# Optimization experiments

Hardware: AMD Instinct MI355X
Metric: run time of the kernel (lower is better)

Reference implementation:

```python
import jax, jax.numpy as jnp
import numpy as np

B, T, D, U = 32, 2048, 1024, 1024

def setup_inputs() -> dict:
    key = jax.random.key(0)
    ks = jax.random.split(key, 8)
    s = 0.02
    return {
        "query": jax.random.normal(ks[0], (B, D), dtype=jnp.float32),
        "values": jax.random.normal(ks[1], (B, T, D), dtype=jnp.float32),
        "W1": jax.random.normal(ks[2], (D, U), dtype=jnp.float32) * s,
        "b1": jnp.zeros((U,), dtype=jnp.float32),
        "W2": jax.random.normal(ks[3], (D, U), dtype=jnp.float32) * s,
        "b2": jnp.zeros((U,), dtype=jnp.float32),
        "V": jax.random.normal(ks[4], (U, 1), dtype=jnp.float32) * s,
        "bv": jnp.zeros((1,), dtype=jnp.float32),
    }

def reference(query, values, W1, b1, W2, b2, V, bv):
    # query: [B, D] -> [B, 1, U] via W2; values: [B, T, D] -> [B, T, U] via W1
    q_proj = query @ W2 + b2                     # [B, U]
    v_proj = jnp.einsum('btd,du->btu', values, W1) + b1   # [B, T, U]
    # score: Dense(1) on tanh(sum) -> [B, T, 1]
    score = jnp.tanh(v_proj + q_proj[:, None, :]) @ V + bv  # [B, T, 1]
    attention_weights = jax.nn.softmax(score, axis=1)        # softmax over time
    context_vector = jnp.sum(attention_weights * values, axis=1)  # [B, D]
    return context_vector, attention_weights
```

## Files before the change

kernel.cpp:

```cpp
#include <hip/hip_runtime.h>
#include <hip/hip_bf16.h>
#include <stdint.h>

#define WS_W1F   0
#define WS_QP2   2097152
#define WS_ESC   (WS_QP2 + 131072)
#define WS_PCTX  (WS_ESC + 262144)
#define WS_PDEN  (WS_PCTX + 4194304)
#define WS_NEED  (WS_PDEN + 4096)

typedef __attribute__((ext_vector_type(8))) short bf16x8;
typedef __attribute__((ext_vector_type(4))) float f32x4;

__device__ inline uint16_t f2b(float f) {
    __hip_bfloat16 h = __float2bfloat16(f);
    return *reinterpret_cast<uint16_t*>(&h);
}

__global__ __launch_bounds__(256) void k_prep(const float* __restrict__ W1,
                                              const float* __restrict__ query,
                                              const float* __restrict__ W2,
                                              const float* __restrict__ b1,
                                              const float* __restrict__ b2,
                                              __hip_bfloat16* __restrict__ W1f,
                                              float* __restrict__ qp2,
                                              float* __restrict__ zctx,
                                              float* __restrict__ zden) {
    __shared__ float qs[1024];
    __shared__ float part[4][64];
    int blk = blockIdx.x, tid = threadIdx.x;
    if (blk < 256) {
        int lane = tid & 63, fi = tid >> 6;
        int l15 = lane & 15, quad = lane >> 4;
        #pragma unroll
        for (int p = 0; p < 2; ++p) {
            int frag = blk * 8 + p * 4 + fi;
            int ut = frag >> 5, ks = frag & 31;
            union { uint16_t h[8]; int4 v; } pk;
            #pragma unroll
            for (int j = 0; j < 8; ++j) {
                float x = W1[(size_t)(ks * 32 + quad * 8 + j) * 1024 + ut * 16 + l15];
                pk.h[j] = f2b(x);
            }
            *(int4*)((char*)W1f + (size_t)frag * 1024 + lane * 16) = pk.v;
        }
    } else {
        int bq = blk - 256;
        int b = bq >> 4, us = bq & 15, u0 = us * 64;
        if (zctx != nullptr && us == 0) {
            *(float4*)(zctx + b * 1024 + tid * 4) = make_float4(0.f, 0.f, 0.f, 0.f);
            if (b == 0 && tid < 32) zden[tid] = 0.f;
        }
        const float* q = query + b * 1024;
        #pragma unroll
        for (int i = 0; i < 4; ++i) qs[i * 256 + tid] = q[i * 256 + tid];
        __syncthreads();
        int ul = tid & 63, g = tid >> 6;
        float a = 0.f;
        const float* w2p = W2 + (size_t)(g * 256) * 1024 + u0 + ul;
        const float* qg = qs + g * 256;
        #pragma unroll 8
        for (int d = 0; d < 256; ++d)
            a += qg[d] * w2p[(size_t)d * 1024];
        part[g][ul] = a;
        __syncthreads();
        if (tid < 64) {
            float r = part[0][tid] + part[1][tid] + part[2][tid] + part[3][tid]
                    + b1[u0 + tid] + b2[u0 + tid];
            qp2[b * 1024 + u0 + tid] = r;
        }
    }
}

__global__ __launch_bounds__(512, 1) void k_score(
        const float* __restrict__ values, const __hip_bfloat16* __restrict__ W1f,
        const float* __restrict__ qp2, const float* __restrict__ V,
        float* __restrict__ escore, float* __restrict__ pctx,
        float* __restrict__ pden, float* __restrict__ ctxa) {
    extern __shared__ char smem[];
    uint16_t* Al = (uint16_t*)smem;
    float* red = (float*)(smem + 131072);

    const int tid = threadIdx.x;
    const int lane = tid & 63, w = tid >> 6;
    const int quad = lane >> 4, l15 = lane & 15;
    const int b = blockIdx.x >> 5, trow0 = (blockIdx.x & 31) << 6;

    const float* Ag = values + (size_t)(b * 2048 + trow0) * 1024;
    #pragma unroll
    for (int i = 0; i < 16; ++i) {
        int id = i * 512 + tid;
        int row = id >> 7, c = id & 127;
        const float* src = Ag + (size_t)row * 1024 + c * 8;
        float4 v0 = *(const float4*)src;
        float4 v1 = *(const float4*)(src + 4);
        union { uint16_t h[8]; int4 v; } pk;
        pk.h[0]=f2b(v0.x); pk.h[1]=f2b(v0.y); pk.h[2]=f2b(v0.z); pk.h[3]=f2b(v0.w);
        pk.h[4]=f2b(v1.x); pk.h[5]=f2b(v1.y); pk.h[6]=f2b(v1.z); pk.h[7]=f2b(v1.w);
        int pos = (c & 112) | ((c & 15) ^ (row & 15));
        *(int4*)(Al + (size_t)row * 1024 + pos * 8) = pk.v;
    }
    __syncthreads();

    const char* Bbase = (const char*)W1f + (size_t)(w * 8) * 32768 + lane * 16;

    f32x4 acc[4][8];
    #pragma unroll
    for (int rt = 0; rt < 4; ++rt)
        #pragma unroll
        for (int ct = 0; ct < 8; ++ct) acc[rt][ct] = (f32x4){0.f, 0.f, 0.f, 0.f};

    bf16x8 af[2][4], bfr[2][8];
    {
        int pos = (quad & 15) ^ l15;
        #pragma unroll
        for (int rt = 0; rt < 4; ++rt)
            af[0][rt] = *(bf16x8*)(Al + (rt * 16 + l15) * 1024 + pos * 8);
        #pragma unroll
        for (int ct = 0; ct < 8; ++ct)
            bfr[0][ct] = *(const bf16x8*)(Bbase + (size_t)(ct * 32) * 1024);
    }

    #pragma unroll 2
    for (int ks = 0; ks < 32; ++ks) {
        const int cur = ks & 1, nxt = cur ^ 1;
        if (ks < 31) {
            int cb = (ks + 1) * 4 + quad;
            int pos = (cb & 112) | ((cb & 15) ^ l15);
            #pragma unroll
            for (int rt = 0; rt < 4; ++rt)
                af[nxt][rt] = *(bf16x8*)(Al + (rt * 16 + l15) * 1024 + pos * 8);
            #pragma unroll
            for (int ct = 0; ct < 4; ++ct)
                bfr[nxt][ct] = *(const bf16x8*)(Bbase + (size_t)(ct * 32 + ks + 1) * 1024);
        }
        __builtin_amdgcn_sched_barrier(0);
        __builtin_amdgcn_s_setprio(1);
        #pragma unroll
        for (int ct = 0; ct < 4; ++ct)
            #pragma unroll
            for (int rt = 0; rt < 4; ++rt)
                acc[rt][ct] = __builtin_amdgcn_mfma_f32_16x16x32_bf16(
                    af[cur][rt], bfr[cur][ct], acc[rt][ct], 0, 0, 0);
        __builtin_amdgcn_s_setprio(0);
        __builtin_amdgcn_sched_barrier(0);
        if (ks < 31) {
            #pragma unroll
            for (int ct = 4; ct < 8; ++ct)
                bfr[nxt][ct] = *(const bf16x8*)(Bbase + (size_t)(ct * 32 + ks + 1) * 1024);
        }
        __builtin_amdgcn_sched_barrier(0);
        __builtin_amdgcn_s_setprio(1);
        #pragma unroll
        for (int ct = 4; ct < 8; ++ct)
            #pragma unroll
            for (int rt = 0; rt < 4; ++rt)
                acc[rt][ct] = __builtin_amdgcn_mfma_f32_16x16x32_bf16(
                    af[cur][rt], bfr[cur][ct], acc[rt][ct], 0, 0, 0);
        __builtin_amdgcn_s_setprio(0);
        __builtin_amdgcn_sched_barrier(0);
    }

    float srow[4][4];
    #pragma unroll
    for (int rt = 0; rt < 4; ++rt)
        #pragma unroll
        for (int r = 0; r < 4; ++r) srow[rt][r] = 0.f;
    #pragma unroll
    for (int ct = 0; ct < 8; ++ct) {
        int u = w * 128 + ct * 16 + l15;
        float qv = qp2[b * 1024 + u];
        float vv = V[u];
        #pragma unroll
        for (int rt = 0; rt < 4; ++rt)
            #pragma unroll
            for (int r = 0; r < 4; ++r) {
                float x = acc[rt][ct][r] + qv;
                float e = __expf(2.f * x);
                float t = 1.f - 2.f * __builtin_amdgcn_rcpf(1.f + e);
                srow[rt][r] += t * vv;
            }
    }

    #pragma unroll
    for (int rt = 0; rt < 4; ++rt)
        #pragma unroll
        for (int r = 0; r < 4; ++r) {
            float s = srow[rt][r];
            s += __shfl_xor(s, 1, 64);
            s += __shfl_xor(s, 2, 64);
            s += __shfl_xor(s, 4, 64);
            s += __shfl_xor(s, 8, 64);
            srow[rt][r] = s;
        }
    if (l15 == 0) {
        #pragma unroll
        for (int rt = 0; rt < 4; ++rt)
            #pragma unroll
            for (int r = 0; r < 4; ++r)
                red[w * 64 + rt * 16 + quad * 4 + r] = srow[rt][r];
    }
    __syncthreads();

    float* wl = (float*)smem;
    if (tid < 64) {
        float s = 0.f;
        #pragma unroll
        for (int k = 0; k < 8; ++k) s += red[k * 64 + tid];
        float e = __expf(s);
        escore[b * 2048 + trow0 + tid] = e;
        wl[tid] = e;
        float dsum = e;
        #pragma unroll
        for (int off = 32; off; off >>= 1) dsum += __shfl_xor(dsum, off, 64);
        if (tid == 0) {
            if (pctx != nullptr) pden[blockIdx.x] = dsum;
            else                 atomicAdd(&pden[b], dsum);
        }
    }
    __syncthreads();

    {
        const float* Vg = values + (size_t)(b * 2048 + trow0) * 1024 + tid * 2;
        float ax = 0.f, ay = 0.f;
        #pragma unroll 8
        for (int t = 0; t < 64; ++t) {
            float wv = wl[t];
            float2 v = *(const float2*)(Vg + (size_t)t * 1024);
            ax += wv * v.x; ay += wv * v.y;
        }
        if (pctx != nullptr) {
            *(float2*)(pctx + (size_t)blockIdx.x * 1024 + tid * 2) = make_float2(ax, ay);
        } else {
            float* o = ctxa + b * 1024 + tid * 2;
            atomicAdd(o + 0, ax);
            atomicAdd(o + 1, ay);
        }
    }
}

__global__ __launch_bounds__(256) void k_final(const float* __restrict__ pctx,
                                               const float* __restrict__ pden,
                                               const float* __restrict__ escore,
                                               float* __restrict__ out) {
    __shared__ float sinv;
    int b = blockIdx.x, tid = threadIdx.x;
    if (tid == 0) {
        float dsum = 0.f;
        if (pctx != nullptr) {
            #pragma unroll
            for (int t = 0; t < 32; ++t) dsum += pden[b * 32 + t];
        } else {
            dsum = pden[b];
        }
        sinv = 1.f / dsum;
    }
    __syncthreads();
    float inv = sinv;

    int d = tid * 4;
    if (pctx != nullptr) {
        float4 a = {0.f, 0.f, 0.f, 0.f};
        #pragma unroll 8
        for (int t = 0; t < 32; ++t) {
            float4 p = *(const float4*)(pctx + (size_t)(b * 32 + t) * 1024 + d);
            a.x += p.x; a.y += p.y; a.z += p.z; a.w += p.w;
        }
        a.x *= inv; a.y *= inv; a.z *= inv; a.w *= inv;
        *(float4*)(out + b * 1024 + d) = a;
    } else {
        float4 a = *(const float4*)(out + b * 1024 + d);
        a.x *= inv; a.y *= inv; a.z *= inv; a.w *= inv;
        *(float4*)(out + b * 1024 + d) = a;
    }

    #pragma unroll
    for (int i = 0; i < 8; ++i) {
        int t = i * 256 + tid;
        out[32768 + b * 2048 + t] = escore[b * 2048 + t] * inv;
    }
}

extern "C" void kernel_launch(void* const* d_in, const int* in_sizes, int n_in,
                              void* d_out, int out_size, void* d_ws, size_t ws_size,
                              hipStream_t stream) {
    const float* query  = (const float*)d_in[0];
    const float* values = (const float*)d_in[1];
    const float* W1 = (const float*)d_in[2];
    const float* b1 = (const float*)d_in[3];
    const float* W2 = (const float*)d_in[4];
    const float* b2 = (const float*)d_in[5];
    const float* V  = (const float*)d_in[6];

    char* ws = (char*)d_ws;
    __hip_bfloat16* W1f = (__hip_bfloat16*)(ws + WS_W1F);
    float* qp2 = (float*)(ws + WS_QP2);
    float* out = (float*)d_out;

    const bool big = ws_size >= (size_t)WS_NEED;
    float* escore = big ? (float*)(ws + WS_ESC)  : out + 32768;
    float* pctx   = big ? (float*)(ws + WS_PCTX) : nullptr;
    float* pden   = big ? (float*)(ws + WS_PDEN) : (float*)(ws + WS_ESC);
    float* zctx   = big ? nullptr : out;
    float* zden   = big ? nullptr : pden;

    (void)hipFuncSetAttribute((const void*)k_score,
                              hipFuncAttributeMaxDynamicSharedMemorySize, 133120);

    k_prep<<<768, 256, 0, stream>>>(W1, query, W2, b1, b2, W1f, qp2, zctx, zden);
    k_score<<<1024, 512, 133120, stream>>>(values, W1f, qp2, V, escore, pctx, pden, out);
    k_final<<<32, 256, 0, stream>>>(pctx, pden, escore, out);
}
```

Measured before the change: 529.0 us.

## Double-buffer values tile in LDS and overlap staging with MFMA loop

Instead of staging the whole 64x1024 values tile into shared memory before the GEMM, the kernel now stages it in four 256-column chunks into two 32KB LDS buffers, loading the next chunk during MFMA compute. Shared memory per block drops from about 130KB to 66KB, which could allow two blocks per CU and overlaps global load latency with compute. The K iteration order is also rotated per block so that concurrent blocks hit different W1 rows. The cost is extra barriers per chunk and more register pressure from holding staged values across MFMA phases.

```diff
diff --git a/kernel.cpp b/kernel.cpp
--- a/kernel.cpp
+++ b/kernel.cpp
@@ -78,87 +78,108 @@
         float* __restrict__ escore, float* __restrict__ pctx,
         float* __restrict__ pden, float* __restrict__ ctxa) {
     extern __shared__ char smem[];
-    uint16_t* Al = (uint16_t*)smem;
-    float* red = (float*)(smem + 131072);
+    float* red = (float*)(smem + 65536);
 
     const int tid = threadIdx.x;
     const int lane = tid & 63, w = tid >> 6;
     const int quad = lane >> 4, l15 = lane & 15;
     const int b = blockIdx.x >> 5, trow0 = (blockIdx.x & 31) << 6;
+    const int rot = blockIdx.x & 7;
 
     const float* Ag = values + (size_t)(b * 2048 + trow0) * 1024;
-    #pragma unroll
-    for (int i = 0; i < 16; ++i) {
-        int id = i * 512 + tid;
-        int row = id >> 7, c = id & 127;
-        const float* src = Ag + (size_t)row * 1024 + c * 8;
-        float4 v0 = *(const float4*)src;
-        float4 v1 = *(const float4*)(src + 4);
+
+    const int crow = tid >> 5, sc = tid & 31;
+    const int pos_w = (sc & 16) | ((sc & 15) ^ crow);
+    const float* sgbase = Ag + (size_t)crow * 1024 + sc * 8;
+    char* wbase = smem + crow * 512 + pos_w * 16;
+
+    const char* Bbase = (const char*)W1f + (size_t)(w * 8) * 32768 + lane * 16;
+
+    f32x4 acc[4][8];
+    #pragma unroll
+    for (int rt = 0; rt < 4; ++rt)
+        #pragma unroll
+        for (int ct = 0; ct < 8; ++ct) acc[rt][ct] = (f32x4){0.f, 0.f, 0.f, 0.f};
+
+    bf16x8 bfr[2][8];
+
+    #pragma unroll
+    for (int s = 0; s < 4; ++s) {
+        float4 v0 = *(const float4*)(sgbase + s * 16384);
+        float4 v1 = *(const float4*)(sgbase + s * 16384 + 4);
         union { uint16_t h[8]; int4 v; } pk;
         pk.h[0]=f2b(v0.x); pk.h[1]=f2b(v0.y); pk.h[2]=f2b(v0.z); pk.h[3]=f2b(v0.w);
         pk.h[4]=f2b(v1.x); pk.h[5]=f2b(v1.y); pk.h[6]=f2b(v1.z); pk.h[7]=f2b(v1.w);
-        int pos = (c & 112) | ((c & 15) ^ (row & 15));
-        *(int4*)(Al + (size_t)row * 1024 + pos * 8) = pk.v;
-    }
-    __syncthreads();
-
-    const char* Bbase = (const char*)W1f + (size_t)(w * 8) * 32768 + lane * 16;
-
-    f32x4 acc[4][8];
-    #pragma unroll
-    for (int rt = 0; rt < 4; ++rt)
-        #pragma unroll
-        for (int ct = 0; ct < 8; ++ct) acc[rt][ct] = (f32x4){0.f, 0.f, 0.f, 0.f};
-
-    bf16x8 af[2][4], bfr[2][8];
-    {
-        int pos = (quad & 15) ^ l15;
-        #pragma unroll
-        for (int rt = 0; rt < 4; ++rt)
-            af[0][rt] = *(bf16x8*)(Al + (rt * 16 + l15) * 1024 + pos * 8);
-        #pragma unroll
-        for (int ct = 0; ct < 8; ++ct)
-            bfr[0][ct] = *(const bf16x8*)(Bbase + (size_t)(ct * 32) * 1024);
-    }
-
-    #pragma unroll 2
-    for (int ks = 0; ks < 32; ++ks) {
-        const int cur = ks & 1, nxt = cur ^ 1;
-        if (ks < 31) {
-            int cb = (ks + 1) * 4 + quad;
-            int pos = (cb & 112) | ((cb & 15) ^ l15);
+        *(int4*)(wbase + s * 8192) = pk.v;
+    }
+    #pragma unroll
+    for (int ct = 0; ct < 8; ++ct)
+        bfr[0][ct] = *(const bf16x8*)(Bbase + (size_t)(ct * 32 + rot) * 1024);
+    asm volatile("s_waitcnt lgkmcnt(0)" ::: "memory");
+    __builtin_amdgcn_s_barrier();
+    __builtin_amdgcn_sched_barrier(0);
+
+    #pragma unroll
+    for (int q = 0; q < 4; ++q) {
+        const int abuf = q & 1;
+        #pragma unroll
+        for (int ksl = 0; ksl < 8; ++ksl) {
+            const int it = q * 8 + ksl;
+            const int curb = it & 1;
+            const bool do_stage = (q < 3) && (ksl < 4);
+            float4 sv0, sv1;
+            if (do_stage) {
+                const float* sp = sgbase + ksl * 16384 + (q + 1) * 256;
+                sv0 = *(const float4*)sp;
+                sv1 = *(const float4*)(sp + 4);
+            }
+            const int lc = (ksl + rot) & 7;
+            const int cbi = lc * 4 + quad;
+            const int posr = (cbi & 16) | ((cbi & 15) ^ l15);
+            bf16x8 af[4];
             #pragma unroll
             for (int rt = 0; rt < 4; ++rt)
-                af[nxt][rt] = *(bf16x8*)(Al + (rt * 16 + l15) * 1024 + pos * 8);
+                af[rt] = *(bf16x8*)(smem + abuf * 32768 + (rt * 16 + l15) * 512 + posr * 16);
+            if (it < 31) {
+                const int nq = (ksl == 7) ? q + 1 : q;
+                const int nlc = (ksl + 1 + rot) & 7;
+                const int nkg = nq * 8 + nlc;
+                #pragma unroll
+                for (int ct = 0; ct < 8; ++ct)
+                    bfr[curb ^ 1][ct] =
+                        *(const bf16x8*)(Bbase + (size_t)(ct * 32 + nkg) * 1024);
+            }
+            __builtin_amdgcn_sched_barrier(0);
+            __builtin_amdgcn_s_setprio(1);
             #pragma unroll
             for (int ct = 0; ct < 4; ++ct)
-                bfr[nxt][ct] = *(const bf16x8*)(Bbase + (size_t)(ct * 32 + ks + 1) * 1024);
-        }
-        __builtin_amdgcn_sched_barrier(0);
-        __builtin_amdgcn_s_setprio(1);
-        #pragma unroll
-        for (int ct = 0; ct < 4; ++ct)
-            #pragma unroll
-            for (int rt = 0; rt < 4; ++rt)
-                acc[rt][ct] = __builtin_amdgcn_mfma_f32_16x16x32_bf16(
-                    af[cur][rt], bfr[cur][ct], acc[rt][ct], 0, 0, 0);
-        __builtin_amdgcn_s_setprio(0);
-        __builtin_amdgcn_sched_barrier(0);
-        if (ks < 31) {
+                #pragma unroll
+                for (int rt = 0; rt < 4; ++rt)
+                    acc[rt][ct] = __builtin_amdgcn_mfma_f32_16x16x32_bf16(
+                        af[rt], bfr[curb][ct], acc[rt][ct], 0, 0, 0);
+            __builtin_amdgcn_s_setprio(0);
+            __builtin_amdgcn_sched_barrier(0);
+            __builtin_amdgcn_s_setprio(1);
             #pragma unroll
             for (int ct = 4; ct < 8; ++ct)
-                bfr[nxt][ct] = *(const bf16x8*)(Bbase + (size_t)(ct * 32 + ks + 1) * 1024);
-        }
-        __builtin_amdgcn_sched_barrier(0);
-        __builtin_amdgcn_s_setprio(1);
-        #pragma unroll
-        for (int ct = 4; ct < 8; ++ct)
-            #pragma unroll
-            for (int rt = 0; rt < 4; ++rt)
-                acc[rt][ct] = __builtin_amdgcn_mfma_f32_16x16x32_bf16(
-                    af[cur][rt], bfr[cur][ct], acc[rt][ct], 0, 0, 0);
-        __builtin_amdgcn_s_setprio(0);
-        __builtin_amdgcn_sched_barrier(0);
+                #pragma unroll
+                for (int rt = 0; rt < 4; ++rt)
+                    acc[rt][ct] = __builtin_amdgcn_mfma_f32_16x16x32_bf16(
+                        af[rt], bfr[curb][ct], acc[rt][ct], 0, 0, 0);
+            __builtin_amdgcn_s_setprio(0);
+            __builtin_amdgcn_sched_barrier(0);
+            if (do_stage) {
+                union { uint16_t h[8]; int4 v; } pk;
+                pk.h[0]=f2b(sv0.x); pk.h[1]=f2b(sv0.y); pk.h[2]=f2b(sv0.z); pk.h[3]=f2b(sv0.w);
+                pk.h[4]=f2b(sv1.x); pk.h[5]=f2b(sv1.y); pk.h[6]=f2b(sv1.z); pk.h[7]=f2b(sv1.w);
+                *(int4*)(wbase + (abuf ^ 1) * 32768 + ksl * 8192) = pk.v;
+            }
+        }
+        if (q < 3) {
+            asm volatile("s_waitcnt lgkmcnt(0)" ::: "memory");
+            __builtin_amdgcn_s_barrier();
+            __builtin_amdgcn_sched_barrier(0);
+        }
     }
 
     float srow[4][4];
@@ -305,9 +326,9 @@
     float* zden   = big ? nullptr : pden;
 
     (void)hipFuncSetAttribute((const void*)k_score,
-                              hipFuncAttributeMaxDynamicSharedMemorySize, 133120);
+                              hipFuncAttributeMaxDynamicSharedMemorySize, 67584);
 
     k_prep<<<768, 256, 0, stream>>>(W1, query, W2, b1, b2, W1f, qp2, zctx, zden);
-    k_score<<<1024, 512, 133120, stream>>>(values, W1f, qp2, V, escore, pctx, pden, out);
+    k_score<<<1024, 512, 67584, stream>>>(values, W1f, qp2, V, escore, pctx, pden, out);
     k_final<<<32, 256, 0, stream>>>(pctx, pden, escore, out);
 }
```

Result: no change. 519.8 us (-1.7%).
